# Kernel tuning notes

Hardware: AMD Instinct MI355X
Metric: run time of the kernel (lower is better)

The kernel has to match this reference:

```python
import jax, jax.numpy as jnp
import numpy as np

B, H, W, C = 128, 8, 32, 512
RNN = 512; EMB = 512; ATT = 512
VOCAB = 110          # vocab_size -> classes = VOCAB + 1
MAXLEN = 30          # loop runs MAXLEN + 1 steps


def setup_inputs() -> dict:
    key = jax.random.key(0)
    ks = jax.random.split(key, 16)
    w = lambda i, shape: jax.random.normal(ks[i], shape, jnp.float32) * 0.02
    return {
        "features": jax.random.normal(ks[0], (B, H, W, C), jnp.float32),
        "holistic": jax.random.normal(ks[1], (B, RNN), jnp.float32),
        "gt": jax.random.randint(ks[2], (B, MAXLEN + 1), 0, VOCAB + 1),
        "embed_W": w(3, (VOCAB + 1, EMB)),
        "k0": w(4, (EMB, 4 * RNN)), "rk0": w(5, (RNN, 4 * RNN)), "b0": jnp.zeros((4 * RNN,), jnp.float32),
        "k1": w(6, (RNN, 4 * RNN)), "rk1": w(7, (RNN, 4 * RNN)), "b1": jnp.zeros((4 * RNN,), jnp.float32),
        "Wh": w(8, (RNN, ATT)),                       # 1x1 conv on (B,1,1,RNN) == dense
        "Wf": w(9, (3, 3, C, ATT)), "bf": jnp.zeros((ATT,), jnp.float32),
        "wa": w(10, (ATT, 1)),                        # 1x1 conv -> scalar attention logit
        "out_W": w(11, (2 * RNN, VOCAB + 1)), "out_b": jnp.zeros((VOCAB + 1,), jnp.float32),
    }


def _lstm(x, h, c, k, rk, b):
    # Keras LSTMCell: gates order i, f, g(cell), o
    z = x @ k + h @ rk + b
    i, f, g, o = jnp.split(z, 4, axis=-1)
    c2 = jax.nn.sigmoid(f) * c + jax.nn.sigmoid(i) * jnp.tanh(g)
    h2 = jax.nn.sigmoid(o) * jnp.tanh(c2)
    return h2, c2


def reference(features, holistic, gt, embed_W, k0, rk0, b0, k1, rk1, b1,
              Wh, Wf, bf, wa, out_W, out_b):
    Bb, Hh, Ww, Cc = features.shape
    # features_projector (3x3 conv, SAME) is timestep-invariant: precompute once
    fproj = jax.lax.conv_general_dilated(
        features, Wf, (1, 1), "SAME",
        dimension_numbers=("NHWC", "HWIO", "NHWC")) + bf          # (B,H,W,ATT)

    zeros = jnp.zeros((Bb, RNN), features.dtype)
    # prime stacked LSTM with holistic vector (zero initial state)
    h0, c0 = _lstm(holistic, zeros, zeros, k0, rk0, b0)
    h1, c1 = _lstm(h0, zeros, zeros, k1, rk1, b1)

    # teacher forcing: step 0 uses SOS token = vocab_size+1 (out-of-range -> zero one-hot),
    # step t>0 uses gt[:, t-1]
    sos = jnp.full((1, Bb), VOCAB + 1, gt.dtype)
    symbols = jnp.concatenate([sos, gt[:, :MAXLEN].T], axis=0)     # (T, B), T = MAXLEN+1

    def step(carry, sym):
        h0, c0, h1, c1 = carry
        x = jax.nn.one_hot(sym, VOCAB + 1, dtype=features.dtype) @ embed_W   # (B, EMB)
        h0, c0 = _lstm(x, h0, c0, k0, rk0, b0)
        h1, c1 = _lstm(h0, h1, c1, k1, rk1, b1)
        # attention over conv feature map
        hp = h1 @ Wh                                               # (B, ATT)
        proj = jnp.tanh(fproj + hp[:, None, None, :])              # (B,H,W,ATT)
        att = (proj @ wa).reshape(Bb, Hh * Ww)                     # (B, H*W)
        att = jax.nn.softmax(att, axis=-1).reshape(Bb, Hh, Ww, 1)
        glimpse = jnp.sum(features * att, axis=(1, 2))             # (B, C)
        logits = jnp.concatenate([h1, glimpse], axis=-1) @ out_W + out_b
        return (h0, c0, h1, c1), logits

    _, logits = jax.lax.scan(step, (h0, c0, h1, c1), symbols)      # (T, B, VOCAB+1)
    return jnp.transpose(logits, (1, 0, 2))                        # (B, T, VOCAB+1)
```

## Files before the change

kernel.cpp:

```cpp
#include <hip/hip_runtime.h>


typedef __bf16 bf16;
typedef bf16 bf16x8 __attribute__((ext_vector_type(8)));
typedef float f32x4 __attribute__((ext_vector_type(4)));

#define MFMA16(a, b, c) __builtin_amdgcn_mfma_f32_16x16x32_bf16((a), (b), (c), 0, 0, 0)

__device__ __forceinline__ float b2f(unsigned short u) {
    return __uint_as_float(((unsigned int)u) << 16);
}
__device__ __forceinline__ unsigned short f2b(float f) {
    unsigned int x = __float_as_uint(f);
    unsigned int r = (x + 0x7fffu + ((x >> 16) & 1u)) >> 16;
    return (unsigned short)r;
}
__device__ __forceinline__ float tanh_fast(float x) {
    const float e = exp2f(2.885390082f * x);
    return 1.0f - 2.0f * __builtin_amdgcn_rcpf(e + 1.0f);
}
__device__ __forceinline__ float sig_fast(float x) {
    return __builtin_amdgcn_rcpf(1.0f + exp2f(-1.44269504f * x));
}
__device__ __forceinline__ void gl16(const ushort* g, ushort* l) {
    __builtin_amdgcn_global_load_lds(
        (const __attribute__((address_space(1))) void*)g,
        (__attribute__((address_space(3))) void*)l, 16, 0, 0);
}

__global__ void detect_dtype(const void* __restrict__ feat, int* __restrict__ flag) {
    if (threadIdx.x == 0 && blockIdx.x == 0) {
        const ushort* u = (const ushort*)feat;
        int cnt = 0;
        for (int i = 0; i < 128; i += 2) {
            const int e = (u[i] >> 7) & 0xFF;
            if (e >= 96 && e <= 150) ++cnt;
        }
        *flag = (cnt >= 40) ? 0 : 1;
    }
}

__global__ __launch_bounds__(256) void cvt_bf16(
    const void* __restrict__ src, ushort* __restrict__ dst, int n,
    const int* __restrict__ flag) {
    const int i = blockIdx.x * 256 + threadIdx.x;
    if (i >= n) return;
    if (*flag) dst[i] = f2b(((const float*)src)[i]);
    else       dst[i] = ((const ushort*)src)[i];
}

__global__ __launch_bounds__(256) void cvt_f32(
    const void* __restrict__ src, float* __restrict__ dst, int n,
    const int* __restrict__ flag) {
    const int i = blockIdx.x * 256 + threadIdx.x;
    if (i >= n) return;
    if (*flag) dst[i] = ((const float*)src)[i];
    else       dst[i] = b2f(((const ushort*)src)[i]);
}

__global__ __launch_bounds__(256) void build_featpad(
    const void* __restrict__ feat, ushort* __restrict__ featPad,
    const int* __restrict__ flag) {
    const int i = blockIdx.x * 256 + threadIdx.x;
    if (i >= 128 * 10 * 34 * 512) return;
    const int c = i & 511;
    const int xy = i >> 9;
    const int x = xy % 34;
    const int t2 = xy / 34;
    const int y = t2 % 10;
    const int b = t2 / 10;
    ushort v = 0;
    if (y >= 1 && y <= 8 && x >= 1 && x <= 32) {
        const size_t si = ((size_t)((b * 8 + y - 1) * 32 + (x - 1)) << 9) + c;
        v = *flag ? f2b(((const float*)feat)[si]) : ((const ushort*)feat)[si];
    }
    featPad[i] = v;
}

__global__ __launch_bounds__(256) void transpose_any(
    const void* __restrict__ in, ushort* __restrict__ out, int R, int C,
    const int* __restrict__ flag) {
    __shared__ float s[32][33];
    const int f32 = *flag;
    const int nbc = C >> 5;
    const int rb = blockIdx.x / nbc, cb = blockIdx.x % nbc;
    const int tx = threadIdx.x & 31, ty = threadIdx.x >> 5;
#pragma unroll
    for (int k = 0; k < 4; ++k) {
        const size_t idx = (size_t)(rb * 32 + ty + k * 8) * C + cb * 32 + tx;
        s[ty + k * 8][tx] = f32 ? ((const float*)in)[idx] : b2f(((const ushort*)in)[idx]);
    }
    __syncthreads();
#pragma unroll
    for (int k = 0; k < 4; ++k)
        out[(size_t)(cb * 32 + ty + k * 8) * R + rb * 32 + tx] = f2b(s[tx][ty + k * 8]);
}

__global__ __launch_bounds__(256) void woT_build(
    const float* __restrict__ outWf, ushort* __restrict__ WoTpad) {
    const int i = blockIdx.x * 256 + threadIdx.x;
    if (i >= 131072) return;
    const int v = i >> 10, k = i & 1023;
    WoTpad[i] = (v < 111) ? f2b(outWf[k * 111 + v]) : (ushort)0;
}

__global__ __launch_bounds__(256) void conv_fproj(
    const ushort* __restrict__ featPad, const ushort* __restrict__ WfT,
    const float* __restrict__ bff, ushort* __restrict__ fproj) {
    __shared__ __align__(16) ushort As[128 * 64];
    __shared__ __align__(16) ushort Bs[128 * 64];
    const int tid = threadIdx.x;
    const int nb = blockIdx.x >> 8;
    const int rb = blockIdx.x & 255;
    const int b = rb >> 1, p0 = (rb & 1) << 7;
    const int w = tid >> 6, lane = tid & 63, l15 = lane & 15, q = lane >> 4;
    const int wr = (w >> 1) << 6, wc = (w & 1) << 6;
    const int chunkoff = (((lane & 7) ^ (lane >> 3)) << 3);
    int aoff[4], boff[4];
#pragma unroll
    for (int i = 0; i < 4; ++i) {
        const int r = w * 32 + (lane >> 3) + i * 8;
        const int p = p0 + r;
        const int yy = p >> 5, xx = p & 31;
        aoff[i] = (((b * 10 + yy) * 34 + xx) << 9) + chunkoff;
        boff[i] = (nb * 128 + r) * 4608 + chunkoff;
    }
    const int swa = l15 & 7;
    f32x4 acc[4][4] = {};
    for (int kb = 0; kb < 72; ++kb) {
        const int tap = kb >> 3;
        const int dy = tap / 3, dx = tap - dy * 3;
        const int koffA = ((dy * 34 + dx) << 9) + ((kb & 7) << 6);
        const int koffB = kb * 64;
        __syncthreads();
#pragma unroll
        for (int i = 0; i < 4; ++i) {
            gl16(featPad + aoff[i] + koffA, &As[(w * 32 + i * 8) * 64]);
            gl16(WfT + boff[i] + koffB, &Bs[(w * 32 + i * 8) * 64]);
        }
        __syncthreads();
#pragma unroll
        for (int ks = 0; ks < 64; ks += 32) {
            const int cq = (ks >> 3) + q;
            const int col = ((cq ^ swa) << 3);
            bf16x8 af[4], bfr[4];
#pragma unroll
            for (int i = 0; i < 4; ++i) af[i] = *(const bf16x8*)&As[(wr + i * 16 + l15) * 64 + col];
#pragma unroll
            for (int j = 0; j < 4; ++j) bfr[j] = *(const bf16x8*)&Bs[(wc + j * 16 + l15) * 64 + col];
#pragma unroll
            for (int i = 0; i < 4; ++i)
#pragma unroll
                for (int j = 0; j < 4; ++j)
                    acc[i][j] = MFMA16(af[i], bfr[j], acc[i][j]);
        }
    }
    const int rowbase = rb * 128 + wr, colbase = nb * 128 + wc;
#pragma unroll
    for (int i = 0; i < 4; ++i)
#pragma unroll
        for (int j = 0; j < 4; ++j)
#pragma unroll
            for (int rr = 0; rr < 4; ++rr) {
                const int row = rowbase + i * 16 + q * 4 + rr;
                const int col = colbase + j * 16 + l15;
                fproj[(size_t)row * 512 + col] = f2b(acc[i][j][rr] + bff[col]);
            }
}

__global__ __launch_bounds__(256) void gemm_bt(
    const ushort* __restrict__ A, const ushort* __restrict__ BT,
    float* __restrict__ C, int M, int N, int K, int lda) {
    __shared__ __align__(16) bf16 As[128][72];
    __shared__ __align__(16) bf16 Bs[128][72];
    const int tid = threadIdx.x;
    const int nnb = N >> 7;
    const int rb = blockIdx.x / nnb, nb = blockIdx.x % nnb;
    const int ar = tid >> 1, ah = (tid & 1) << 5;
    const int w = tid >> 6, lane = tid & 63, l15 = lane & 15, q = lane >> 4;
    const int wr = (w >> 1) << 6, wc = (w & 1) << 6;
    const int r_glob = rb * 128 + ar;
    const bool aval = (r_glob < M);
    const int r_ld = aval ? r_glob : 0;
    f32x4 acc[4][4] = {};
    const int nkb = K >> 6;
    for (int kb = 0; kb < nkb; ++kb) {
        const uint4 z4 = {0u, 0u, 0u, 0u};
        const uint4* asrc = (const uint4*)(A + (size_t)r_ld * lda + kb * 64 + ah);
        uint4 a0 = asrc[0], a1 = asrc[1], a2 = asrc[2], a3 = asrc[3];
        if (!aval) { a0 = z4; a1 = z4; a2 = z4; a3 = z4; }
        const uint4* bsrc = (const uint4*)(BT + (size_t)(nb * 128 + ar) * K + kb * 64 + ah);
        uint4 b0v = bsrc[0], b1v = bsrc[1], b2v = bsrc[2], b3v = bsrc[3];
        __syncthreads();
        *(uint4*)&As[ar][ah] = a0;
        *(uint4*)&As[ar][ah + 8] = a1;
        *(uint4*)&As[ar][ah + 16] = a2;
        *(uint4*)&As[ar][ah + 24] = a3;
        *(uint4*)&Bs[ar][ah] = b0v;
        *(uint4*)&Bs[ar][ah + 8] = b1v;
        *(uint4*)&Bs[ar][ah + 16] = b2v;
        *(uint4*)&Bs[ar][ah + 24] = b3v;
        __syncthreads();
#pragma unroll
        for (int ks = 0; ks < 64; ks += 32) {
            bf16x8 af[4], bfr[4];
#pragma unroll
            for (int i = 0; i < 4; ++i) af[i] = *(const bf16x8*)&As[wr + i * 16 + l15][ks + q * 8];
#pragma unroll
            for (int j = 0; j < 4; ++j) bfr[j] = *(const bf16x8*)&Bs[wc + j * 16 + l15][ks + q * 8];
#pragma unroll
            for (int i = 0; i < 4; ++i)
#pragma unroll
                for (int j = 0; j < 4; ++j)
                    acc[i][j] = MFMA16(af[i], bfr[j], acc[i][j]);
        }
    }
#pragma unroll
    for (int i = 0; i < 4; ++i)
#pragma unroll
        for (int j = 0; j < 4; ++j)
#pragma unroll
            for (int rr = 0; rr < 4; ++rr) {
                const int row = rb * 128 + wr + i * 16 + q * 4 + rr;
                const int col = nb * 128 + wc + j * 16 + l15;
                if (row < M) C[(size_t)row * N + col] = acc[i][j][rr];
            }
}

__global__ __launch_bounds__(256) void lstm_stage(
    int t,
    const ushort* __restrict__ holistic, const int* __restrict__ gt,
    const float* __restrict__ b0f, const float* __restrict__ b1f,
    const ushort* __restrict__ k0T, const ushort* __restrict__ rk0T,
    const ushort* __restrict__ k1T, const ushort* __restrict__ rk1T,
    const float* __restrict__ E0,
    ushort* h0b0, ushort* h0b1, ushort* h1b0, ushort* h1b1,
    float* c0buf, float* c1buf, ushort* HG) {
    const int part = blockIdx.x >> 7;
    const int bi = blockIdx.x & 127;
    const ushort *A1 = nullptr, *A2 = nullptr, *B1 = nullptr, *B2 = nullptr;
    const float* bias = nullptr;
    ushort *hout = nullptr, *hout2 = nullptr;
    float* cbuf = nullptr;
    bool useC = false, useE = false;
    if (part == 0) {
        if (!(t == -2 || (t >= 0 && t <= 30))) return;
        bias = b0f; cbuf = c0buf;
        if (t == -2) { A1 = holistic; B1 = k0T; hout = h0b1; }
        else {
            A1 = ((t + 1) & 1) ? h0b1 : h0b0;
            B1 = rk0T;
            hout = (t & 1) ? h0b1 : h0b0;
            useC = true; useE = true;
        }
    } else {
        if (!(t == -1 || (t >= 1 && t <= 31))) return;
        bias = b1f; cbuf = c1buf;
        if (t == -1) { A1 = h0b1; B1 = k1T; hout = h1b1; }
        else {
            const int s = t - 1;
            A1 = (s & 1) ? h0b1 : h0b0;
            A2 = ((s + 1) & 1) ? h1b1 : h1b0;
            B1 = k1T; B2 = rk1T;
            hout = (s & 1) ? h1b1 : h1b0;
            hout2 = HG + (size_t)s * 131072;
            useC = true;
        }
    }
    const int m0 = (bi >> 5) << 5;
    const int cc0 = (bi & 31) << 4;
    const int tid = threadIdx.x;
    const int w = tid >> 6, lane = tid & 63, l15 = lane & 15, q = lane >> 4;
    __shared__ __align__(16) ushort As1[32 * 520];
    __shared__ __align__(16) ushort As2[32 * 520];
    __shared__ float zs[4][32][17];
#pragma unroll
    for (int it = 0; it < 8; ++it) {
        const int idx = tid + it * 256;
        const int row = idx >> 6, chv = idx & 63;
        *(uint4*)&As1[row * 520 + chv * 8] =
            *(const uint4*)(A1 + (size_t)(m0 + row) * 512 + chv * 8);
    }
    if (A2) {
#pragma unroll
        for (int it = 0; it < 8; ++it) {
            const int idx = tid + it * 256;
            const int row = idx >> 6, chv = idx & 63;
            *(uint4*)&As2[row * 520 + chv * 8] =
                *(const uint4*)(A2 + (size_t)(m0 + row) * 512 + chv * 8);
        }
    }
    __syncthreads();
    const int nkb = A2 ? 16 : 8;
    const size_t brow = (size_t)(w * 512 + cc0 + l15) * 512 + q * 8;
    auto bp = [&](int kb) -> const ushort* {
        const ushort* base = (kb < 8) ? B1 : B2;
        return base + brow + (kb & 7) * 64;
    };
    bf16x8 c0v = *(const bf16x8*)bp(0);
    bf16x8 c1v = *(const bf16x8*)(bp(0) + 32);
    bf16x8 n0v = *(const bf16x8*)bp(1);
    bf16x8 n1v = *(const bf16x8*)(bp(1) + 32);
    f32x4 acc0 = {}, acc1 = {};
    for (int kb = 0; kb < nkb; ++kb) {
        const bf16x8 p0 = c0v, p1 = c1v;
        c0v = n0v; c1v = n1v;
        if (kb + 2 < nkb) {
            n0v = *(const bf16x8*)bp(kb + 2);
            n1v = *(const bf16x8*)(bp(kb + 2) + 32);
        }
        const ushort* asrc = (kb < 8) ? As1 : As2;
        const int kk = (kb & 7) * 64 + q * 8;
        bf16x8 a00 = *(const bf16x8*)&asrc[l15 * 520 + kk];
        bf16x8 a10 = *(const bf16x8*)&asrc[(16 + l15) * 520 + kk];
        bf16x8 a01 = *(const bf16x8*)&asrc[l15 * 520 + kk + 32];
        bf16x8 a11 = *(const bf16x8*)&asrc[(16 + l15) * 520 + kk + 32];
        acc0 = MFMA16(a00, p0, acc0);
        acc1 = MFMA16(a10, p0, acc1);
        acc0 = MFMA16(a01, p1, acc0);
        acc1 = MFMA16(a11, p1, acc1);
    }
#pragma unroll
    for (int rr = 0; rr < 4; ++rr) {
        zs[w][q * 4 + rr][l15] = acc0[rr];
        zs[w][16 + q * 4 + rr][l15] = acc1[rr];
    }
    __syncthreads();
#pragma unroll
    for (int it = 0; it < 2; ++it) {
        const int e = tid + it * 256;
        const int mm = e >> 4, cc = e & 15;
        const int brow2 = m0 + mm, col = cc0 + cc;
        float zi = zs[0][mm][cc] + bias[col];
        float zf = zs[1][mm][cc] + bias[512 + col];
        float zg = zs[2][mm][cc] + bias[1024 + col];
        float zo = zs[3][mm][cc] + bias[1536 + col];
        if (useE) {
            const int s = (t == 0) ? 111 : gt[brow2 * 31 + t - 1];
            if (s >= 0 && s < 111) {
                const float* er = E0 + (size_t)s * 2048;
                zi += er[col]; zf += er[512 + col]; zg += er[1024 + col]; zo += er[1536 + col];
            }
        }
        const float cp = useC ? cbuf[brow2 * 512 + col] : 0.0f;
        const float c2 = sig_fast(zf) * cp + sig_fast(zi) * tanh_fast(zg);
        const float h = sig_fast(zo) * tanh_fast(c2);
        cbuf[brow2 * 512 + col] = c2;
        hout[brow2 * 512 + col] = f2b(h);
        if (hout2) hout2[brow2 * 1024 + col] = f2b(h);
    }
}

__global__ __launch_bounds__(256) void att_logits(
    const ushort* __restrict__ fproj, const float* __restrict__ HP,
    const float* __restrict__ waf, float* __restrict__ attL) {
    __shared__ float hpS[16][512];
    __shared__ float waS[512];
    __shared__ float accS[128][17];
    const int tid = threadIdx.x;
    const int b = blockIdx.x >> 2, ph = (blockIdx.x >> 1) & 1, th = blockIdx.x & 1;
    const int t0 = th << 4, tc = th ? 15 : 16;
    const int pl = tid & 127, ch = tid >> 7;
    const int p = ph * 128 + pl;
    for (int i = tid; i < 16 * 512; i += 256) {
        const int tt = i >> 9, c = i & 511;
        hpS[tt][c] = (tt < tc) ? HP[((size_t)(t0 + tt) * 128 + b) * 512 + c] : 0.0f;
    }
    waS[tid] = waf[tid];
    if (tid < 256) waS[256 + tid] = waf[256 + tid];
    __syncthreads();
    float acc[16];
#pragma unroll
    for (int tt = 0; tt < 16; ++tt) acc[tt] = 0.f;
    const ushort* frow = fproj + (size_t)(b * 256 + p) * 512 + ch * 256;
    for (int c8 = 0; c8 < 32; ++c8) {
        const int cc = ch * 256 + c8 * 8;
        const uint4 fv = *(const uint4*)(frow + c8 * 8);
        float f[8];
        f[0] = b2f((unsigned short)(fv.x & 0xffff)); f[1] = b2f((unsigned short)(fv.x >> 16));
        f[2] = b2f((unsigned short)(fv.y & 0xffff)); f[3] = b2f((unsigned short)(fv.y >> 16));
        f[4] = b2f((unsigned short)(fv.z & 0xffff)); f[5] = b2f((unsigned short)(fv.z >> 16));
        f[6] = b2f((unsigned short)(fv.w & 0xffff)); f[7] = b2f((unsigned short)(fv.w >> 16));
        float w8[8];
#pragma unroll
        for (int j = 0; j < 8; ++j) w8[j] = waS[cc + j];
#pragma unroll
        for (int tt = 0; tt < 16; ++tt) {
            const float* hp8 = &hpS[tt][cc];
            float s = 0.f;
#pragma unroll
            for (int j = 0; j < 8; ++j)
                s += tanh_fast(f[j] + hp8[j]) * w8[j];
            acc[tt] += s;
        }
    }
    if (ch == 1) {
#pragma unroll
        for (int tt = 0; tt < 16; ++tt) accS[pl][tt] = acc[tt];
    }
    __syncthreads();
    if (ch == 0) {
        for (int tt = 0; tt < tc; ++tt)
            attL[((size_t)(t0 + tt) * 128 + b) * 256 + p] = acc[tt] + accS[pl][tt];
    }
}

__global__ __launch_bounds__(256) void glimpse_kernel(
    const ushort* __restrict__ featPad, const float* __restrict__ attL,
    ushort* __restrict__ HG) {
    __shared__ float attS[31][256];
    const int tid = threadIdx.x;
    const int b = blockIdx.x >> 1, chh = blockIdx.x & 1;
    const int c0 = chh << 8;
    const int w = tid >> 6, lane = tid & 63;
    for (int i = tid; i < 31 * 256; i += 256) {
        const int tt = i >> 8, p = i & 255;
        attS[tt][p] = attL[((size_t)tt * 128 + b) * 256 + p];
    }
    __syncthreads();
    for (int tt = w; tt < 31; tt += 4) {
        float v0 = attS[tt][lane], v1 = attS[tt][lane + 64];
        float v2 = attS[tt][lane + 128], v3 = attS[tt][lane + 192];
        float mx = fmaxf(fmaxf(v0, v1), fmaxf(v2, v3));
#pragma unroll
        for (int m = 1; m < 64; m <<= 1) mx = fmaxf(mx, __shfl_xor(mx, m));
        const float e0 = expf(v0 - mx), e1 = expf(v1 - mx);
        const float e2 = expf(v2 - mx), e3 = expf(v3 - mx);
        float s = e0 + e1 + e2 + e3;
#pragma unroll
        for (int m = 1; m < 64; m <<= 1) s += __shfl_xor(s, m);
        const float r = 1.0f / s;
        attS[tt][lane] = e0 * r;  attS[tt][lane + 64] = e1 * r;
        attS[tt][lane + 128] = e2 * r;  attS[tt][lane + 192] = e3 * r;
    }
    __syncthreads();
    float acc[31];
#pragma unroll
    for (int tt = 0; tt < 31; ++tt) acc[tt] = 0.f;
    for (int p = 0; p < 256; ++p) {
        const size_t fi = (((size_t)(b * 10 + (p >> 5) + 1) * 34 + (p & 31) + 1) << 9) + c0 + tid;
        const float fv = b2f(featPad[fi]);
#pragma unroll
        for (int tt = 0; tt < 31; ++tt) acc[tt] += fv * attS[tt][p];
    }
#pragma unroll
    for (int tt = 0; tt < 31; ++tt)
        HG[((size_t)tt * 128 + b) * 1024 + 512 + c0 + tid] = f2b(acc[tt]);
}

__global__ __launch_bounds__(256) void logits_store(
    const float* __restrict__ C, const float* __restrict__ outBf,
    void* __restrict__ out, const int* __restrict__ flag) {
    const int i = blockIdx.x * 256 + threadIdx.x;
    if (i >= 3968 * 111) return;
    const int r = i / 111, v = i - r * 111;
    const int tt = r >> 7, b = r & 127;
    const float a = C[(size_t)r * 128 + v] + outBf[v];
    const size_t oi = ((size_t)b * 31 + tt) * 111 + v;
    if (*flag) ((float*)out)[oi] = a;
    else       ((ushort*)out)[oi] = f2b(a);
}

extern "C" void kernel_launch(void* const* d_in, const int* in_sizes, int n_in,
                              void* d_out, int out_size, void* d_ws, size_t ws_size,
                              hipStream_t stream) {
    (void)in_sizes; (void)n_in; (void)out_size;
    const void* features = d_in[0];
    const void* holistic = d_in[1];
    const int*  gt       = (const int*)d_in[2];
    const void* embed_W  = d_in[3];
    const void* k0 = d_in[4];
    const void* rk0 = d_in[5];
    const void* b0 = d_in[6];
    const void* k1 = d_in[7];
    const void* rk1 = d_in[8];
    const void* b1 = d_in[9];
    const void* Wh = d_in[10];
    const void* Wf = d_in[11];
    const void* bfv = d_in[12];
    const void* wa = d_in[13];
    const void* outW = d_in[14];
    const void* outB = d_in[15];

    char* ws = (char*)d_ws;
    size_t off = 0;
    auto take = [&](size_t bytes) -> char* {
        char* p = ws + off;
        off += (bytes + 255) & ~(size_t)255;
        return p;
    };
    int*    flag    = (int*)take(256);
    ushort* featPad = (ushort*)take(128ull * 10 * 34 * 512 * 2);
    ushort* holB  = (ushort*)take(65536ull * 2);
    ushort* embB  = (ushort*)take(56832ull * 2);
    float*  b0f   = (float*)take(2048ull * 4);
    float*  b1f   = (float*)take(2048ull * 4);
    float*  bff   = (float*)take(512ull * 4);
    float*  waf   = (float*)take(512ull * 4);
    float*  outBf = (float*)take(111ull * 4);
    float*  outWf = (float*)take(113664ull * 4);
    ushort* fproj = (ushort*)take(32768ull * 512 * 2);
    ushort* WfT   = (ushort*)take(4608ull * 512 * 2);
    ushort* k0T   = (ushort*)take(2048ull * 512 * 2);
    ushort* rk0T  = (ushort*)take(2048ull * 512 * 2);
    ushort* k1T   = (ushort*)take(2048ull * 512 * 2);
    ushort* rk1T  = (ushort*)take(2048ull * 512 * 2);
    ushort* WhT   = (ushort*)take(512ull * 512 * 2);
    float*  E0    = (float*)take(111ull * 2048 * 4);
    ushort* h0b0  = (ushort*)take(128ull * 512 * 2);
    ushort* h0b1  = (ushort*)take(128ull * 512 * 2);
    ushort* h1b0  = (ushort*)take(128ull * 512 * 2);
    ushort* h1b1  = (ushort*)take(128ull * 512 * 2);
    float*  c0buf = (float*)take(128ull * 512 * 4);
    float*  c1buf = (float*)take(128ull * 512 * 4);
    ushort* HG    = (ushort*)take(3968ull * 1024 * 2);
    float*  HP    = (float*)take(3968ull * 512 * 4);
    float*  attL  = (float*)take(31ull * 128 * 256 * 4);
    float*  Cout   = (float*)attL;
    ushort* WoTpad = (ushort*)((char*)attL + 3968ull * 128 * 4);
    if (off > ws_size) return;

    detect_dtype<<<dim3(1), dim3(64), 0, stream>>>(features, flag);
    build_featpad<<<dim3(87040), dim3(256), 0, stream>>>(features, featPad, flag);
    cvt_bf16<<<dim3(256), dim3(256), 0, stream>>>(holistic, holB, 65536, flag);
    cvt_bf16<<<dim3(222), dim3(256), 0, stream>>>(embed_W, embB, 56832, flag);
    cvt_f32<<<dim3(8), dim3(256), 0, stream>>>(b0, b0f, 2048, flag);
    cvt_f32<<<dim3(8), dim3(256), 0, stream>>>(b1, b1f, 2048, flag);
    cvt_f32<<<dim3(2), dim3(256), 0, stream>>>(bfv, bff, 512, flag);
    cvt_f32<<<dim3(2), dim3(256), 0, stream>>>(wa, waf, 512, flag);
    cvt_f32<<<dim3(1), dim3(256), 0, stream>>>(outB, outBf, 111, flag);
    cvt_f32<<<dim3(444), dim3(256), 0, stream>>>(outW, outWf, 113664, flag);
    transpose_any<<<dim3(16 * 64), dim3(256), 0, stream>>>(k0, k0T, 512, 2048, flag);
    transpose_any<<<dim3(16 * 64), dim3(256), 0, stream>>>(rk0, rk0T, 512, 2048, flag);
    transpose_any<<<dim3(16 * 64), dim3(256), 0, stream>>>(k1, k1T, 512, 2048, flag);
    transpose_any<<<dim3(16 * 64), dim3(256), 0, stream>>>(rk1, rk1T, 512, 2048, flag);
    transpose_any<<<dim3(16 * 16), dim3(256), 0, stream>>>(Wh, WhT, 512, 512, flag);
    transpose_any<<<dim3(144 * 16), dim3(256), 0, stream>>>(Wf, WfT, 4608, 512, flag);
    conv_fproj<<<dim3(1024), dim3(256), 0, stream>>>(featPad, WfT, bff, fproj);
    gemm_bt<<<dim3(16), dim3(256), 0, stream>>>(embB, k0T, E0, 111, 2048, 512, 512);
    for (int t = -2; t <= 31; ++t)
        lstm_stage<<<dim3(256), dim3(256), 0, stream>>>(t, holB, gt, b0f, b1f,
            k0T, rk0T, k1T, rk1T, E0, h0b0, h0b1, h1b0, h1b1, c0buf, c1buf, HG);
    gemm_bt<<<dim3(31 * 4), dim3(256), 0, stream>>>(HG, WhT, HP, 3968, 512, 512, 1024);
    att_logits<<<dim3(512), dim3(256), 0, stream>>>(fproj, HP, waf, attL);
    glimpse_kernel<<<dim3(256), dim3(256), 0, stream>>>(featPad, attL, HG);
    woT_build<<<dim3(512), dim3(256), 0, stream>>>(outWf, WoTpad);
    gemm_bt<<<dim3(31), dim3(256), 0, stream>>>(HG, WoTpad, Cout, 3968, 128, 1024, 1024);
    logits_store<<<dim3(1721), dim3(256), 0, stream>>>(Cout, outBf, d_out, flag);
}
```

Baseline: 995.9 us.

## Use raw v_exp, fold tanh scaling into attention weights, transpose glimpse attention layout

Replaces exp2f with a raw v_exp_f32 inline asm in the tanh and sigmoid helpers and in the softmax. In the attention-logit kernel, tanh(x)*w is rewritten as w - 2w/(e^{2x}+1): the 2*log2(e) scale is folded into the features and hidden projections, and the constant sum of w is added once at the end, which removes per-element multiplies and adds. The glimpse kernel now stores attention as position-major with a padded stride, so the inner loop reads 31 weights with float4 LDS loads. The LSTM GEMM deepens its B-operand register prefetch from two stages to three. Raw v_exp skips range handling for denormals, which may slightly change accuracy.

```diff
diff --git a/kernel.cpp b/kernel.cpp
--- a/kernel.cpp
+++ b/kernel.cpp
@@ -15,12 +15,17 @@
     unsigned int r = (x + 0x7fffu + ((x >> 16) & 1u)) >> 16;
     return (unsigned short)r;
 }
+__device__ __forceinline__ float exp2_raw(float x) {
+    float r;
+    asm("v_exp_f32 %0, %1" : "=v"(r) : "v"(x));
+    return r;
+}
 __device__ __forceinline__ float tanh_fast(float x) {
-    const float e = exp2f(2.885390082f * x);
+    const float e = exp2_raw(2.885390082f * x);
     return 1.0f - 2.0f * __builtin_amdgcn_rcpf(e + 1.0f);
 }
 __device__ __forceinline__ float sig_fast(float x) {
-    return __builtin_amdgcn_rcpf(1.0f + exp2f(-1.44269504f * x));
+    return __builtin_amdgcn_rcpf(1.0f + exp2_raw(-1.44269504f * x));
 }
 __device__ __forceinline__ void gl16(const ushort* g, ushort* l) {
     __builtin_amdgcn_global_load_lds(
@@ -297,17 +302,16 @@
         const ushort* base = (kb < 8) ? B1 : B2;
         return base + brow + (kb & 7) * 64;
     };
-    bf16x8 c0v = *(const bf16x8*)bp(0);
-    bf16x8 c1v = *(const bf16x8*)(bp(0) + 32);
-    bf16x8 n0v = *(const bf16x8*)bp(1);
-    bf16x8 n1v = *(const bf16x8*)(bp(1) + 32);
+    bf16x8 b0a = *(const bf16x8*)bp(0), b1a = *(const bf16x8*)(bp(0) + 32);
+    bf16x8 b0b = *(const bf16x8*)bp(1), b1b = *(const bf16x8*)(bp(1) + 32);
+    bf16x8 b0c = *(const bf16x8*)bp(2), b1c = *(const bf16x8*)(bp(2) + 32);
     f32x4 acc0 = {}, acc1 = {};
     for (int kb = 0; kb < nkb; ++kb) {
-        const bf16x8 p0 = c0v, p1 = c1v;
-        c0v = n0v; c1v = n1v;
-        if (kb + 2 < nkb) {
-            n0v = *(const bf16x8*)bp(kb + 2);
-            n1v = *(const bf16x8*)(bp(kb + 2) + 32);
+        const bf16x8 p0 = b0a, p1 = b1a;
+        b0a = b0b; b1a = b1b; b0b = b0c; b1b = b1c;
+        if (kb + 3 < nkb) {
+            b0c = *(const bf16x8*)bp(kb + 3);
+            b1c = *(const bf16x8*)(bp(kb + 3) + 32);
         }
         const ushort* asrc = (kb < 8) ? As1 : As2;
         const int kk = (kb & 7) * 64 + q * 8;
@@ -364,11 +368,20 @@
     const int p = ph * 128 + pl;
     for (int i = tid; i < 16 * 512; i += 256) {
         const int tt = i >> 9, c = i & 511;
-        hpS[tt][c] = (tt < tc) ? HP[((size_t)(t0 + tt) * 128 + b) * 512 + c] : 0.0f;
-    }
-    waS[tid] = waf[tid];
-    if (tid < 256) waS[256 + tid] = waf[256 + tid];
-    __syncthreads();
+        hpS[tt][c] = (tt < tc) ? 2.885390082f * HP[((size_t)(t0 + tt) * 128 + b) * 512 + c] : 0.0f;
+    }
+    waS[tid] = -2.0f * waf[tid];
+    if (tid < 256) waS[256 + tid] = -2.0f * waf[256 + tid];
+    __syncthreads();
+    float sumW = 0.f;
+    {
+        const float* wh = &waS[ch * 256];
+        for (int c4 = 0; c4 < 64; ++c4) {
+            const float4 wv = *(const float4*)&wh[c4 * 4];
+            sumW += wv.x + wv.y + wv.z + wv.w;
+        }
+        sumW *= -0.5f;
+    }
     float acc[16];
 #pragma unroll
     for (int tt = 0; tt < 16; ++tt) acc[tt] = 0.f;
@@ -381,57 +394,66 @@
         f[2] = b2f((unsigned short)(fv.y & 0xffff)); f[3] = b2f((unsigned short)(fv.y >> 16));
         f[4] = b2f((unsigned short)(fv.z & 0xffff)); f[5] = b2f((unsigned short)(fv.z >> 16));
         f[6] = b2f((unsigned short)(fv.w & 0xffff)); f[7] = b2f((unsigned short)(fv.w >> 16));
-        float w8[8];
-#pragma unroll
-        for (int j = 0; j < 8; ++j) w8[j] = waS[cc + j];
+#pragma unroll
+        for (int j = 0; j < 8; ++j) f[j] *= 2.885390082f;
+        const float4 w0 = *(const float4*)&waS[cc];
+        const float4 w1 = *(const float4*)&waS[cc + 4];
 #pragma unroll
         for (int tt = 0; tt < 16; ++tt) {
-            const float* hp8 = &hpS[tt][cc];
-            float s = 0.f;
-#pragma unroll
-            for (int j = 0; j < 8; ++j)
-                s += tanh_fast(f[j] + hp8[j]) * w8[j];
-            acc[tt] += s;
+            const float4 h0 = *(const float4*)&hpS[tt][cc];
+            const float4 h1 = *(const float4*)&hpS[tt][cc + 4];
+            float s = acc[tt];
+            s = fmaf(__builtin_amdgcn_rcpf(exp2_raw(f[0] + h0.x) + 1.0f), w0.x, s);
+            s = fmaf(__builtin_amdgcn_rcpf(exp2_raw(f[1] + h0.y) + 1.0f), w0.y, s);
+            s = fmaf(__builtin_amdgcn_rcpf(exp2_raw(f[2] + h0.z) + 1.0f), w0.z, s);
+            s = fmaf(__builtin_amdgcn_rcpf(exp2_raw(f[3] + h0.w) + 1.0f), w0.w, s);
+            s = fmaf(__builtin_amdgcn_rcpf(exp2_raw(f[4] + h1.x) + 1.0f), w1.x, s);
+            s = fmaf(__builtin_amdgcn_rcpf(exp2_raw(f[5] + h1.y) + 1.0f), w1.y, s);
+            s = fmaf(__builtin_amdgcn_rcpf(exp2_raw(f[6] + h1.z) + 1.0f), w1.z, s);
+            s = fmaf(__builtin_amdgcn_rcpf(exp2_raw(f[7] + h1.w) + 1.0f), w1.w, s);
+            acc[tt] = s;
         }
     }
     if (ch == 1) {
 #pragma unroll
-        for (int tt = 0; tt < 16; ++tt) accS[pl][tt] = acc[tt];
+        for (int tt = 0; tt < 16; ++tt) accS[pl][tt] = acc[tt] + sumW;
     }
     __syncthreads();
     if (ch == 0) {
         for (int tt = 0; tt < tc; ++tt)
-            attL[((size_t)(t0 + tt) * 128 + b) * 256 + p] = acc[tt] + accS[pl][tt];
+            attL[((size_t)(t0 + tt) * 128 + b) * 256 + p] = acc[tt] + sumW + accS[pl][tt];
     }
 }
 
 __global__ __launch_bounds__(256) void glimpse_kernel(
     const ushort* __restrict__ featPad, const float* __restrict__ attL,
     ushort* __restrict__ HG) {
-    __shared__ float attS[31][256];
+    __shared__ __align__(16) float attT[256 * 36];
     const int tid = threadIdx.x;
     const int b = blockIdx.x >> 1, chh = blockIdx.x & 1;
     const int c0 = chh << 8;
     const int w = tid >> 6, lane = tid & 63;
     for (int i = tid; i < 31 * 256; i += 256) {
         const int tt = i >> 8, p = i & 255;
-        attS[tt][p] = attL[((size_t)tt * 128 + b) * 256 + p];
+        attT[p * 36 + tt] = attL[((size_t)tt * 128 + b) * 256 + p];
     }
     __syncthreads();
     for (int tt = w; tt < 31; tt += 4) {
-        float v0 = attS[tt][lane], v1 = attS[tt][lane + 64];
-        float v2 = attS[tt][lane + 128], v3 = attS[tt][lane + 192];
+        float v0 = attT[lane * 36 + tt], v1 = attT[(lane + 64) * 36 + tt];
+        float v2 = attT[(lane + 128) * 36 + tt], v3 = attT[(lane + 192) * 36 + tt];
         float mx = fmaxf(fmaxf(v0, v1), fmaxf(v2, v3));
 #pragma unroll
         for (int m = 1; m < 64; m <<= 1) mx = fmaxf(mx, __shfl_xor(mx, m));
-        const float e0 = expf(v0 - mx), e1 = expf(v1 - mx);
-        const float e2 = expf(v2 - mx), e3 = expf(v3 - mx);
+        const float e0 = exp2_raw((v0 - mx) * 1.44269504f);
+        const float e1 = exp2_raw((v1 - mx) * 1.44269504f);
+        const float e2 = exp2_raw((v2 - mx) * 1.44269504f);
+        const float e3 = exp2_raw((v3 - mx) * 1.44269504f);
         float s = e0 + e1 + e2 + e3;
 #pragma unroll
         for (int m = 1; m < 64; m <<= 1) s += __shfl_xor(s, m);
         const float r = 1.0f / s;
-        attS[tt][lane] = e0 * r;  attS[tt][lane + 64] = e1 * r;
-        attS[tt][lane + 128] = e2 * r;  attS[tt][lane + 192] = e3 * r;
+        attT[lane * 36 + tt] = e0 * r;  attT[(lane + 64) * 36 + tt] = e1 * r;
+        attT[(lane + 128) * 36 + tt] = e2 * r;  attT[(lane + 192) * 36 + tt] = e3 * r;
     }
     __syncthreads();
     float acc[31];
@@ -440,8 +462,30 @@
     for (int p = 0; p < 256; ++p) {
         const size_t fi = (((size_t)(b * 10 + (p >> 5) + 1) * 34 + (p & 31) + 1) << 9) + c0 + tid;
         const float fv = b2f(featPad[fi]);
-#pragma unroll
-        for (int tt = 0; tt < 31; ++tt) acc[tt] += fv * attS[tt][p];
+        const float4 a0 = *(const float4*)&attT[p * 36];
+        const float4 a1 = *(const float4*)&attT[p * 36 + 4];
+        const float4 a2 = *(const float4*)&attT[p * 36 + 8];
+        const float4 a3 = *(const float4*)&attT[p * 36 + 12];
+        const float4 a4 = *(const float4*)&attT[p * 36 + 16];
+        const float4 a5 = *(const float4*)&attT[p * 36 + 20];
+        const float4 a6 = *(const float4*)&attT[p * 36 + 24];
+        const float4 a7 = *(const float4*)&attT[p * 36 + 28];
+        acc[0] = fmaf(fv, a0.x, acc[0]);   acc[1] = fmaf(fv, a0.y, acc[1]);
+        acc[2] = fmaf(fv, a0.z, acc[2]);   acc[3] = fmaf(fv, a0.w, acc[3]);
+        acc[4] = fmaf(fv, a1.x, acc[4]);   acc[5] = fmaf(fv, a1.y, acc[5]);
+        acc[6] = fmaf(fv, a1.z, acc[6]);   acc[7] = fmaf(fv, a1.w, acc[7]);
+        acc[8] = fmaf(fv, a2.x, acc[8]);   acc[9] = fmaf(fv, a2.y, acc[9]);
+        acc[10] = fmaf(fv, a2.z, acc[10]); acc[11] = fmaf(fv, a2.w, acc[11]);
+        acc[12] = fmaf(fv, a3.x, acc[12]); acc[13] = fmaf(fv, a3.y, acc[13]);
+        acc[14] = fmaf(fv, a3.z, acc[14]); acc[15] = fmaf(fv, a3.w, acc[15]);
+        acc[16] = fmaf(fv, a4.x, acc[16]); acc[17] = fmaf(fv, a4.y, acc[17]);
+        acc[18] = fmaf(fv, a4.z, acc[18]); acc[19] = fmaf(fv, a4.w, acc[19]);
+        acc[20] = fmaf(fv, a5.x, acc[20]); acc[21] = fmaf(fv, a5.y, acc[21]);
+        acc[22] = fmaf(fv, a5.z, acc[22]); acc[23] = fmaf(fv, a5.w, acc[23]);
+        acc[24] = fmaf(fv, a6.x, acc[24]); acc[25] = fmaf(fv, a6.y, acc[25]);
+        acc[26] = fmaf(fv, a6.z, acc[26]); acc[27] = fmaf(fv, a6.w, acc[27]);
+        acc[28] = fmaf(fv, a7.x, acc[28]); acc[29] = fmaf(fv, a7.y, acc[29]);
+        acc[30] = fmaf(fv, a7.z, acc[30]);
     }
 #pragma unroll
     for (int tt = 0; tt < 31; ++tt)
```

New measurement: 933.4 us. 6.3% less time.
